# Optimization experiments

Measured on AMD Instinct MI355X. Metric: run time of the kernel, lower is better.

Reference implementation:

```python
import jax, jax.numpy as jnp
import numpy as np

B = 64          # graphs per batch
N = 1500        # nodes per graph (equal sizes -> vectorized sortpool)
NT = B * N      # total nodes
DEG = 16        # avg in-degree
E_PER = N * DEG # edges per graph
F_IN = 128
K = 30          # sortpool k
LATENT = [32, 32, 32, 1]  # total 97
TOTAL_LAT = sum(LATENT)
OUT_DIM = 128


def setup_inputs() -> dict:
    key = jax.random.key(0)
    ks = jax.random.split(key, 16)
    node_feat = jax.random.normal(ks[0], (NT, F_IN), dtype=jnp.float32)
    # edges constrained within each graph (block-diagonal adjacency)
    offs = (jnp.arange(B, dtype=jnp.int32) * N)[:, None]
    edge_src = (jax.random.randint(ks[1], (B, E_PER), 0, N, dtype=jnp.int32) + offs).reshape(-1)
    edge_dst = (jax.random.randint(ks[2], (B, E_PER), 0, N, dtype=jnp.int32) + offs).reshape(-1)

    def lin(k, fan_in, shape):
        return jax.random.normal(k, shape, dtype=jnp.float32) * (1.0 / np.sqrt(fan_in))

    inp = dict(node_feat=node_feat, edge_src=edge_src, edge_dst=edge_dst)
    dims = [F_IN] + LATENT
    for i in range(4):
        inp[f'W{i+1}'] = lin(ks[3 + i], dims[i], (dims[i], dims[i + 1]))
        inp[f'b{i+1}'] = jnp.zeros((dims[i + 1],), jnp.float32)
    inp['conv1_w'] = lin(ks[8], TOTAL_LAT, (16, TOTAL_LAT))   # Conv1d(1,16,97,stride=97)
    inp['conv1_b'] = jnp.zeros((16,), jnp.float32)
    inp['conv2_w'] = lin(ks[9], 16 * 5, (32, 16, 5))          # Conv1d(16,32,5)
    inp['conv2_b'] = jnp.zeros((32,), jnp.float32)
    inp['out_w'] = lin(ks[10], 352, (352, OUT_DIM))
    inp['out_b'] = jnp.zeros((OUT_DIM,), jnp.float32)
    return inp


def reference(node_feat, edge_src, edge_dst, W1, b1, W2, b2, W3, b3, W4, b4,
              conv1_w, conv1_b, conv2_w, conv2_b, out_w, out_b):
    # node degrees (+1 for self loop), from in-edges
    deg = jax.ops.segment_sum(jnp.ones_like(edge_dst, jnp.float32), edge_dst, num_segments=NT)
    node_degs = (deg + 1.0)[:, None]

    # 4 graph-conv layers: (A @ h + h) -> Linear -> /deg -> tanh, concat features
    h = node_feat
    layers = []
    for W, b in ((W1, b1), (W2, b2), (W3, b3), (W4, b4)):
        agg = jax.ops.segment_sum(h[edge_src], edge_dst, num_segments=NT) + h
        h = jnp.tanh((agg @ W + b) / node_degs)
        layers.append(h)
    feat = jnp.concatenate(layers, axis=1)  # [NT, 97]

    # sortpooling: top-k nodes per graph by the last channel
    sort_ch = feat[:, -1].reshape(B, N)
    _, idx = jax.lax.top_k(sort_ch, K)                    # [B, K]
    gidx = (idx + (jnp.arange(B, dtype=idx.dtype) * N)[:, None]).reshape(-1)
    pooled = feat[gidx].reshape(B, K, TOTAL_LAT)          # [B, K, 97]

    # Conv1d(1,16,97,stride=97) over flattened [B,1,K*97] == per-slot linear
    c1 = jax.nn.relu(jnp.einsum('bkd,od->bok', pooled, conv1_w) + conv1_b[None, :, None])  # [B,16,K]
    mp = c1.reshape(B, 16, K // 2, 2).max(axis=-1)        # MaxPool1d(2,2) -> [B,16,15]
    c2 = jax.lax.conv_general_dilated(mp, conv2_w, (1,), 'VALID',
                                      dimension_numbers=('NCH', 'OIH', 'NCH'))
    c2 = jax.nn.relu(c2 + conv2_b[None, :, None])         # [B,32,11]
    dense = c2.reshape(B, -1)                             # [B,352]
    return jax.nn.relu(dense @ out_w + out_b)             # relu(relu(x)) == relu(x)
```

## Files before the change

### kernel.cpp

```cpp
#include <hip/hip_runtime.h>

constexpr int B = 64, N = 1500, NT = B * N;
constexpr int E_PER = 24000, E_TOT = B * E_PER;
constexpr int E_PAD = 34560;
constexpr int F_INN = 128, K = 30, TOT = 97;
constexpr int NB_G = 47;
constexpr int GEMM_TILES = NT / 128;
constexpr int GEMM_BLKS = (GEMM_TILES + 3) / 4;

__global__ __launch_bounds__(1024) void prep(const int* __restrict__ src, const int* __restrict__ dst,
                                             ushort* __restrict__ csr, int* __restrict__ rowst,
                                             int* __restrict__ degi, float* __restrict__ degf,
                                             float* __restrict__ tA,
                                             const float* __restrict__ nf, const float* __restrict__ W1) {
    __shared__ union {
        struct { int hist[N]; uint csr_l32[E_PAD / 2]; int wsum[4]; } c;
        struct { float hs[4][32][128]; float Ws[32][32]; } g;
    } u;
    int bid = blockIdx.x, t = threadIdx.x;

    if (bid < B) {
        ushort* csr_l = (ushort*)u.c.csr_l32;
        int g = bid;
        int gbase = g * N;
        const int* dstg = dst + (size_t)g * E_PER;
        const int* srcg = src + (size_t)g * E_PER;

        for (int i = t; i < N; i += 1024) u.c.hist[i] = 0;
        __syncthreads();
        for (int e = t; e < E_PER; e += 1024)
            atomicAdd(&u.c.hist[dstg[e] - gbase], 1);
        __syncthreads();

        int local[6];
        int sum = 0, x = 0;
        if (t < 256) {
#pragma unroll
            for (int i = 0; i < 6; ++i) {
                int v = t * 6 + i;
                int d = (v < N) ? u.c.hist[v] : 0;
                local[i] = d;
                sum += (d + 7) & ~7;
            }
            x = sum;
            int lane = t & 63;
#pragma unroll
            for (int m = 1; m < 64; m <<= 1) {
                int y = __shfl_up(x, m, 64);
                if (lane >= m) x += y;
            }
            if (lane == 63) u.c.wsum[t >> 6] = x;
        }
        __syncthreads();
        if (t < 256) {
            int woff = 0;
            int wv = t >> 6;
            for (int w = 0; w < wv; ++w) woff += u.c.wsum[w];
            int run = x - sum + woff;
#pragma unroll
            for (int i = 0; i < 6; ++i) {
                int v = t * 6 + i;
                if (v < N) {
                    rowst[gbase + v] = g * E_PAD + run;
                    degi[gbase + v] = local[i];
                    degf[gbase + v] = (float)(local[i] + 1);
                    u.c.hist[v] = run;
                    run += (local[i] + 7) & ~7;
                }
            }
        }
        __syncthreads();
        for (int e = t; e < E_PER; e += 1024) {
            int d = dstg[e] - gbase;
            int pos = atomicAdd(&u.c.hist[d], 1);
            csr_l[pos] = (ushort)(srcg[e] - gbase);
        }
        __syncthreads();
        for (int v = t; v < N; v += 1024)
            for (int s = u.c.hist[v]; s & 7; ++s) csr_l[s] = (ushort)v;
        __syncthreads();
        uint* cg = (uint*)(csr + (size_t)g * E_PAD);
        for (int i = t; i < E_PAD / 2; i += 1024)
            cg[i] = u.c.csr_l32[i];
    } else {
        int sub = t >> 8, tid = t & 255;
        int tile = (bid - B) * 4 + sub;
        bool valid = tile < GEMM_TILES;
        int wv = tid >> 6, lane = tid & 63;
        int v0 = tile * 128;
        int og = wv * 8;
        float acc[2][8];
#pragma unroll
        for (int i = 0; i < 2; ++i)
#pragma unroll
            for (int j = 0; j < 8; ++j) acc[i][j] = 0.f;

        for (int kc = 0; kc < F_INN; kc += 32) {
            __syncthreads();
            if (valid) {
                int n = tid >> 1, kh = (tid & 1) * 16;
                const float* hp = nf + (size_t)(v0 + n) * F_INN + kc + kh;
                const float4* hp4 = reinterpret_cast<const float4*>(hp);
                float4 a = hp4[0], b = hp4[1], c = hp4[2], d = hp4[3];
                float (*hs)[128] = u.g.hs[sub];
                hs[kh + 0][n] = a.x;  hs[kh + 1][n] = a.y;  hs[kh + 2][n] = a.z;  hs[kh + 3][n] = a.w;
                hs[kh + 4][n] = b.x;  hs[kh + 5][n] = b.y;  hs[kh + 6][n] = b.z;  hs[kh + 7][n] = b.w;
                hs[kh + 8][n] = c.x;  hs[kh + 9][n] = c.y;  hs[kh + 10][n] = c.z; hs[kh + 11][n] = c.w;
                hs[kh + 12][n] = d.x; hs[kh + 13][n] = d.y; hs[kh + 14][n] = d.z; hs[kh + 15][n] = d.w;
            }
            if (sub == 0) {
                int r = tid >> 3, c4 = (tid & 7) * 4;
                float4 w = *reinterpret_cast<const float4*>(W1 + (size_t)(kc + r) * 32 + c4);
                *reinterpret_cast<float4*>(&u.g.Ws[r][c4]) = w;
            }
            __syncthreads();
            if (valid) {
#pragma unroll
                for (int k = 0; k < 32; ++k) {
                    float2 hv = *reinterpret_cast<const float2*>(&u.g.hs[sub][k][2 * lane]);
                    float4 w0 = *reinterpret_cast<const float4*>(&u.g.Ws[k][og]);
                    float4 w1 = *reinterpret_cast<const float4*>(&u.g.Ws[k][og + 4]);
                    acc[0][0] += hv.x * w0.x; acc[0][1] += hv.x * w0.y; acc[0][2] += hv.x * w0.z; acc[0][3] += hv.x * w0.w;
                    acc[0][4] += hv.x * w1.x; acc[0][5] += hv.x * w1.y; acc[0][6] += hv.x * w1.z; acc[0][7] += hv.x * w1.w;
                    acc[1][0] += hv.y * w0.x; acc[1][1] += hv.y * w0.y; acc[1][2] += hv.y * w0.z; acc[1][3] += hv.y * w0.w;
                    acc[1][4] += hv.y * w1.x; acc[1][5] += hv.y * w1.y; acc[1][6] += hv.y * w1.z; acc[1][7] += hv.y * w1.w;
                }
            }
        }
        if (valid) {
#pragma unroll
            for (int i = 0; i < 2; ++i) {
                float* op = tA + (size_t)(v0 + 2 * lane + i) * 32 + og;
                float4 r0 = {acc[i][0], acc[i][1], acc[i][2], acc[i][3]};
                float4 r1 = {acc[i][4], acc[i][5], acc[i][6], acc[i][7]};
                reinterpret_cast<float4*>(op)[0] = r0;
                reinterpret_cast<float4*>(op)[1] = r1;
            }
        }
    }
}

template <int FUSE>
__global__ __launch_bounds__(256) void agg_f(const float* __restrict__ t,
                                             const ushort* __restrict__ csr, const int* __restrict__ rowst,
                                             const int* __restrict__ degi, const float* __restrict__ degf,
                                             const float* __restrict__ bias, const float* __restrict__ Wn,
                                             float* __restrict__ hout, float* __restrict__ tn) {
    __shared__ float Ws[1024];
    __shared__ float outs[32][32];
    if (FUSE == 32) {
        for (int i = threadIdx.x; i < 1024; i += 256) Ws[i] = Wn[i];
    }
    int bid = blockIdx.x;
    int xcd = bid & 7, j = bid >> 3;
    int g = xcd + 8 * (j / NB_G);
    int nb = j % NB_G;
    int nl = threadIdx.x >> 3;
    int f4 = threadIdx.x & 7;
    int vl = nb * 32 + nl;
    bool valid = vl < N;
    int v = g * N + vl;
    int gb8 = g * N * 8;
    const float4* t4v = reinterpret_cast<const float4*>(t);
    float4 out = {0.f, 0.f, 0.f, 0.f};
    if (valid) {
        float4 tself = t4v[(unsigned)(v * 8 + f4)];
        int e0 = rowst[v];
        int dc = degi[v];
        int pc = (dc + 7) & ~7;
        float scale = (float)(1 + dc - pc);
        float4 acc = {scale * tself.x, scale * tself.y, scale * tself.z, scale * tself.w};
        float4 s1 = {0.f, 0.f, 0.f, 0.f}, s2 = {0.f, 0.f, 0.f, 0.f};
        float4 s3 = {0.f, 0.f, 0.f, 0.f}, s4v = {0.f, 0.f, 0.f, 0.f};
        for (int e = 0; e < pc; e += 8) {
            ushort4 ia = *reinterpret_cast<const ushort4*>(csr + e0 + e);
            ushort4 ib = *reinterpret_cast<const ushort4*>(csr + e0 + e + 4);
            float4 x0 = t4v[(unsigned)(gb8 + ia.x * 8 + f4)];
            float4 x1 = t4v[(unsigned)(gb8 + ia.y * 8 + f4)];
            float4 x2 = t4v[(unsigned)(gb8 + ia.z * 8 + f4)];
            float4 x3 = t4v[(unsigned)(gb8 + ia.w * 8 + f4)];
            float4 x4 = t4v[(unsigned)(gb8 + ib.x * 8 + f4)];
            float4 x5 = t4v[(unsigned)(gb8 + ib.y * 8 + f4)];
            float4 x6 = t4v[(unsigned)(gb8 + ib.z * 8 + f4)];
            float4 x7 = t4v[(unsigned)(gb8 + ib.w * 8 + f4)];
            s1.x += x0.x + x1.x; s1.y += x0.y + x1.y; s1.z += x0.z + x1.z; s1.w += x0.w + x1.w;
            s2.x += x2.x + x3.x; s2.y += x2.y + x3.y; s2.z += x2.z + x3.z; s2.w += x2.w + x3.w;
            s3.x += x4.x + x5.x; s3.y += x4.y + x5.y; s3.z += x4.z + x5.z; s3.w += x4.w + x5.w;
            s4v.x += x6.x + x7.x; s4v.y += x6.y + x7.y; s4v.z += x6.z + x7.z; s4v.w += x6.w + x7.w;
        }
        acc.x += (s1.x + s2.x) + (s3.x + s4v.x);
        acc.y += (s1.y + s2.y) + (s3.y + s4v.y);
        acc.z += (s1.z + s2.z) + (s3.z + s4v.z);
        acc.w += (s1.w + s2.w) + (s3.w + s4v.w);
        float4 bv = *reinterpret_cast<const float4*>(bias + f4 * 4);
        float inv = 1.0f / degf[v];
        out.x = tanhf((acc.x + bv.x) * inv);
        out.y = tanhf((acc.y + bv.y) * inv);
        out.z = tanhf((acc.z + bv.z) * inv);
        out.w = tanhf((acc.w + bv.w) * inv);
        reinterpret_cast<float4*>(hout)[(unsigned)(v * 8 + f4)] = out;
    }
    if (FUSE == 32) {
        *reinterpret_cast<float4*>(&outs[nl][f4 * 4]) = out;
        __syncthreads();
        if (valid) {
            float4 s = {0.f, 0.f, 0.f, 0.f};
#pragma unroll
            for (int ff = 0; ff < 32; ++ff) {
                float h = outs[nl][ff];
                float4 wr = *reinterpret_cast<const float4*>(&Ws[ff * 32 + f4 * 4]);
                s.x += h * wr.x; s.y += h * wr.y; s.z += h * wr.z; s.w += h * wr.w;
            }
            reinterpret_cast<float4*>(tn)[(unsigned)(v * 8 + f4)] = s;
        }
    } else if (valid) {
        float4 w4 = *reinterpret_cast<const float4*>(Wn + f4 * 4);
        float p = out.x * w4.x + out.y * w4.y + out.z * w4.z + out.w * w4.w;
        p += __shfl_xor(p, 4, 64);
        p += __shfl_xor(p, 2, 64);
        p += __shfl_xor(p, 1, 64);
        if (f4 == 0) tn[v] = p;
    }
}

__global__ __launch_bounds__(512) void sort_head(const float* __restrict__ hc1, const float* __restrict__ hc2,
                                                 const float* __restrict__ hc3, const float* __restrict__ t4,
                                                 const ushort* __restrict__ csr, const int* __restrict__ rowst,
                                                 const int* __restrict__ degi, const float* __restrict__ degf,
                                                 const float* __restrict__ b4,
                                                 const float* __restrict__ c1w, const float* __restrict__ c1b,
                                                 const float* __restrict__ c2w, const float* __restrict__ c2b,
                                                 const float* __restrict__ ow, const float* __restrict__ ob,
                                                 float* __restrict__ out) {
    __shared__ float ts[N];
    __shared__ unsigned int svals[N];
    __shared__ float fvals[N];
    __shared__ int hist[2048];
    __shared__ int canA[N], canB[N];
    __shared__ int winners[32];
    __shared__ int wsum[8];
    __shared__ int st_need, st_ncand, st_tb, st_cab, st_nwin;
    __shared__ int topk_s[K];
    __shared__ float pooled[K][TOT];
    __shared__ float c1[16][K];
    __shared__ float mp[16][16];
    __shared__ float dense[352];
    __shared__ float part[4][128];

    int g = blockIdx.x, t = threadIdx.x;
    int gbase = g * N;
    int lane = t & 63, w = t >> 6;

    for (int v = t; v < N; v += 512) ts[v] = t4[gbase + v];
    if (t == 0) { st_need = K; st_nwin = 0; }
    __syncthreads();
    {
        float b4v = b4[0];
        for (int v = t; v < N; v += 512) {
            int gv = gbase + v;
            int e0 = rowst[gv], dc = degi[gv];
            int pc = (dc + 7) & ~7;
            float scale = (float)(1 + dc - pc);
            float a0 = 0.f, a1 = 0.f, a2 = 0.f, a3 = 0.f;
            for (int e = 0; e < pc; e += 4) {
                ushort4 s4 = *reinterpret_cast<const ushort4*>(csr + e0 + e);
                a0 += ts[s4.x];
                a1 += ts[s4.y];
                a2 += ts[s4.z];
                a3 += ts[s4.w];
            }
            float h = tanhf((scale * ts[v] + (a0 + a1) + (a2 + a3) + b4v) / degf[gv]);
            fvals[v] = h;
            unsigned int b = __float_as_uint(h);
            svals[v] = (b & 0x80000000u) ? ~b : (b | 0x80000000u);
        }
    }
    __syncthreads();

    auto mkkey = [&](int idx) {
        return ((unsigned long long)svals[idx] << 31) | (unsigned int)(0x7FFFFFFF - idx);
    };

    const int SHIFTS[6] = {52, 41, 30, 19, 8, 0};
    int curN = N;
    int src = 0;
    for (int pass = 0; pass < 6; ++pass) {
        int shift = SHIFTS[pass];
        int mask = (pass == 5) ? 0xFF : 0x7FF;
        for (int i = t; i < 2048; i += 512) hist[i] = 0;
        if (t == 0) st_ncand = 0;
        __syncthreads();
        for (int i = t; i < curN; i += 512) {
            int idx = (src == 0) ? i : (src == 1 ? canA[i] : canB[i]);
            int d = (int)((mkkey(idx) >> shift) & mask);
            atomicAdd(&hist[d], 1);
        }
        __syncthreads();
        int need = st_need;
        int c[4];
        int s = 0;
#pragma unroll
        for (int u = 0; u < 4; ++u) { c[u] = hist[2047 - (4 * t + u)]; s += c[u]; }
        int x = s;
#pragma unroll
        for (int m = 1; m < 64; m <<= 1) {
            int y = __shfl_up(x, m, 64);
            if (lane >= m) x += y;
        }
        if (lane == 63) wsum[w] = x;
        __syncthreads();
        int woff = 0;
        for (int ww = 0; ww < w; ++ww) woff += wsum[ww];
        int A = woff + x - s;
#pragma unroll
        for (int u = 0; u < 4; ++u) {
            if (A < need && need <= A + c[u]) { st_tb = 2047 - (4 * t + u); st_cab = A; }
            A += c[u];
        }
        __syncthreads();
        int tb = st_tb, cab = st_cab;
        int* dst = (src == 1) ? canB : canA;
        for (int i = t; i < curN; i += 512) {
            int idx = (src == 0) ? i : (src == 1 ? canA[i] : canB[i]);
            int d = (int)((mkkey(idx) >> shift) & mask);
            if (d > tb) {
                int p = atomicAdd(&st_nwin, 1);
                winners[p] = idx;
            } else if (d == tb) {
                int p = atomicAdd(&st_ncand, 1);
                dst[p] = idx;
            }
        }
        __syncthreads();
        int ncand = st_ncand;
        need -= cab;
        if (t == 0) st_need = need;
        if (ncand == need) {
            int base = st_nwin;
            for (int i = t; i < ncand; i += 512) winners[base + i] = dst[i];
            __syncthreads();
            break;
        }
        curN = ncand;
        src = (src == 1) ? 2 : 1;
        __syncthreads();
    }

    if (t < 64) {
        unsigned long long key = (t < K) ? mkkey(winners[t]) : 0ull;
        unsigned long long kk = ~key;
#pragma unroll
        for (int k = 2; k <= 64; k <<= 1) {
#pragma unroll
            for (int j = k >> 1; j > 0; j >>= 1) {
                unsigned long long o = __shfl_xor(kk, j, 64);
                bool keepMin = ((t & j) == 0) == ((t & k) == 0);
                kk = keepMin ? (kk < o ? kk : o) : (kk > o ? kk : o);
            }
        }
        key = ~kk;
        if (t < K) topk_s[t] = 0x7FFFFFFF - (int)(unsigned int)(key & 0x7FFFFFFFu);
    }
    __syncthreads();

    for (int i = t; i < K * TOT; i += 512) {
        int k = i / TOT, d = i % TOT;
        int vloc = topk_s[k];
        int gi = gbase + vloc;
        float val = (d < 32) ? hc1[(size_t)gi * 32 + d]
                  : (d < 64) ? hc2[(size_t)gi * 32 + d - 32]
                  : (d < 96) ? hc3[(size_t)gi * 32 + d - 64]
                             : fvals[vloc];
        pooled[k][d] = val;
    }
    __syncthreads();
    for (int i = t; i < 16 * K; i += 512) {
        int o = i / K, k = i % K;
        float s = c1b[o];
        for (int d = 0; d < TOT; ++d) s += pooled[k][d] * c1w[o * TOT + d];
        c1[o][k] = fmaxf(s, 0.f);
    }
    __syncthreads();
    for (int i = t; i < 16 * 15; i += 512) {
        int o = i / 15, p = i % 15;
        mp[o][p] = fmaxf(c1[o][2 * p], c1[o][2 * p + 1]);
    }
    __syncthreads();
    for (int i = t; i < 352; i += 512) {
        int o = i / 11, p = i % 11;
        float s = c2b[o];
#pragma unroll
        for (int ci = 0; ci < 16; ++ci)
#pragma unroll
            for (int tt = 0; tt < 5; ++tt)
                s += mp[ci][p + tt] * c2w[(o * 16 + ci) * 5 + tt];
        dense[i] = fmaxf(s, 0.f);
    }
    __syncthreads();
    {
        int o = t & 127, q = t >> 7;
        float s = 0.f;
        for (int m = q * 88; m < (q + 1) * 88; ++m) s += dense[m] * ow[m * 128 + o];
        part[q][o] = s;
    }
    __syncthreads();
    if (t < 128) {
        float s = (part[0][t] + part[1][t]) + (part[2][t] + part[3][t]) + ob[t];
        out[g * 128 + t] = fmaxf(s, 0.f);
    }
}

extern "C" void kernel_launch(void* const* d_in, const int* in_sizes, int n_in,
                              void* d_out, int out_size, void* d_ws, size_t ws_size,
                              hipStream_t stream) {
    const float* node_feat = (const float*)d_in[0];
    const int* esrc = (const int*)d_in[1];
    const int* edst = (const int*)d_in[2];
    const float* W1 = (const float*)d_in[3];
    const float* b1 = (const float*)d_in[4];
    const float* W2 = (const float*)d_in[5];
    const float* b2 = (const float*)d_in[6];
    const float* W3 = (const float*)d_in[7];
    const float* b3 = (const float*)d_in[8];
    const float* W4 = (const float*)d_in[9];
    const float* b4 = (const float*)d_in[10];
    const float* c1w = (const float*)d_in[11];
    const float* c1b = (const float*)d_in[12];
    const float* c2w = (const float*)d_in[13];
    const float* c2b = (const float*)d_in[14];
    const float* ow = (const float*)d_in[15];
    const float* ob = (const float*)d_in[16];

    char* ws = (char*)d_ws;
    size_t off = 0;
    auto alloc = [&](size_t bytes) {
        size_t r = off;
        off += (bytes + 255) & ~(size_t)255;
        return r;
    };
    int* deg_i = (int*)(ws + alloc((size_t)NT * 4));
    int* rowst = (int*)(ws + alloc((size_t)NT * 4));
    float* degf = (float*)(ws + alloc((size_t)NT * 4));
    ushort* csr = (ushort*)(ws + alloc((size_t)B * E_PAD * 2));
    float* tA = (float*)(ws + alloc((size_t)NT * 32 * 4));
    float* tB = (float*)(ws + alloc((size_t)NT * 32 * 4));
    float* hc1 = (float*)(ws + alloc((size_t)NT * 32 * 4));
    float* hc2 = (float*)(ws + alloc((size_t)NT * 32 * 4));
    float* hc3 = (float*)(ws + alloc((size_t)NT * 32 * 4));
    float* t4 = (float*)(ws + alloc((size_t)NT * 4));

    prep<<<B + GEMM_BLKS, 1024, 0, stream>>>(esrc, edst, csr, rowst, deg_i, degf,
                                             tA, node_feat, W1);

    agg_f<32><<<8 * NB_G * 8, 256, 0, stream>>>(tA, csr, rowst, deg_i, degf, b1, W2, hc1, tB);
    agg_f<32><<<8 * NB_G * 8, 256, 0, stream>>>(tB, csr, rowst, deg_i, degf, b2, W3, hc2, tA);
    agg_f<1><<<8 * NB_G * 8, 256, 0, stream>>>(tA, csr, rowst, deg_i, degf, b3, W4, hc3, t4);

    sort_head<<<B, 512, 0, stream>>>(hc1, hc2, hc3, t4, csr, rowst, deg_i, degf, b4,
                                     c1w, c1b, c2w, c2b, ow, ob, (float*)d_out);
}
```

Baseline: 117.2 us.

## Split per-graph CSR build into four node-range quarters per block

The CSR construction in prep now uses four blocks per graph, each owning a quarter of the destination nodes. Every block scans the whole edge list with int4 loads and keeps only edges whose destination falls in its range. This gives four times as many CSR-building blocks and a smaller shared-memory footprint per block, so the serial CSR phase should no longer dominate prep. In exchange, each graph's edge list is read four times, and each quarter's padded slice must fit a fixed capacity of 9216, which risks overflow if a quarter's degree total is skewed.

```diff
diff --git a/kernel.cpp b/kernel.cpp
--- a/kernel.cpp
+++ b/kernel.cpp
@@ -2,7 +2,8 @@
 
 constexpr int B = 64, N = 1500, NT = B * N;
 constexpr int E_PER = 24000, E_TOT = B * E_PER;
-constexpr int E_PAD = 34560;
+constexpr int NQ = 4, NPQ = N / NQ;
+constexpr int CAP = 9216;
 constexpr int F_INN = 128, K = 30, TOT = 97;
 constexpr int NB_G = 47;
 constexpr int GEMM_TILES = NT / 128;
@@ -14,31 +15,38 @@
                                              float* __restrict__ tA,
                                              const float* __restrict__ nf, const float* __restrict__ W1) {
     __shared__ union {
-        struct { int hist[N]; uint csr_l32[E_PAD / 2]; int wsum[4]; } c;
+        struct { int hist[NPQ]; uint4 slice[CAP / 8]; int wtot; } c;
         struct { float hs[4][32][128]; float Ws[32][32]; } g;
     } u;
     int bid = blockIdx.x, t = threadIdx.x;
 
-    if (bid < B) {
-        ushort* csr_l = (ushort*)u.c.csr_l32;
-        int g = bid;
-        int gbase = g * N;
-        const int* dstg = dst + (size_t)g * E_PER;
-        const int* srcg = src + (size_t)g * E_PER;
-
-        for (int i = t; i < N; i += 1024) u.c.hist[i] = 0;
-        __syncthreads();
-        for (int e = t; e < E_PER; e += 1024)
-            atomicAdd(&u.c.hist[dstg[e] - gbase], 1);
-        __syncthreads();
-
-        int local[6];
+    if (bid < B * NQ) {
+        ushort* csr_l = (ushort*)u.c.slice;
+        int g = bid >> 2, q = bid & 3;
+        int gbase = g * N, qlo = q * NPQ;
+        const int4* d4 = reinterpret_cast<const int4*>(dst + (size_t)g * E_PER);
+        const int4* s4 = reinterpret_cast<const int4*>(src + (size_t)g * E_PER);
+
+        for (int i = t; i < NPQ; i += 1024) u.c.hist[i] = 0;
+        __syncthreads();
+        for (int i = t; i < E_PER / 4; i += 1024) {
+            int4 d = d4[i];
+            int x0 = d.x - gbase - qlo, x1 = d.y - gbase - qlo;
+            int x2 = d.z - gbase - qlo, x3 = d.w - gbase - qlo;
+            if ((unsigned)x0 < (unsigned)NPQ) atomicAdd(&u.c.hist[x0], 1);
+            if ((unsigned)x1 < (unsigned)NPQ) atomicAdd(&u.c.hist[x1], 1);
+            if ((unsigned)x2 < (unsigned)NPQ) atomicAdd(&u.c.hist[x2], 1);
+            if ((unsigned)x3 < (unsigned)NPQ) atomicAdd(&u.c.hist[x3], 1);
+        }
+        __syncthreads();
+
+        int local[3];
         int sum = 0, x = 0;
-        if (t < 256) {
-#pragma unroll
-            for (int i = 0; i < 6; ++i) {
-                int v = t * 6 + i;
-                int d = (v < N) ? u.c.hist[v] : 0;
+        if (t < 128) {
+#pragma unroll
+            for (int i = 0; i < 3; ++i) {
+                int v = t * 3 + i;
+                int d = (v < NPQ) ? u.c.hist[v] : 0;
                 local[i] = d;
                 sum += (d + 7) & ~7;
             }
@@ -49,42 +57,47 @@
                 int y = __shfl_up(x, m, 64);
                 if (lane >= m) x += y;
             }
-            if (lane == 63) u.c.wsum[t >> 6] = x;
-        }
-        __syncthreads();
-        if (t < 256) {
-            int woff = 0;
-            int wv = t >> 6;
-            for (int w = 0; w < wv; ++w) woff += u.c.wsum[w];
-            int run = x - sum + woff;
-#pragma unroll
-            for (int i = 0; i < 6; ++i) {
-                int v = t * 6 + i;
-                if (v < N) {
-                    rowst[gbase + v] = g * E_PAD + run;
-                    degi[gbase + v] = local[i];
-                    degf[gbase + v] = (float)(local[i] + 1);
+        }
+        if (t == 63) u.c.wtot = x;
+        __syncthreads();
+        if (t < 128) {
+            int base = (t >= 64) ? u.c.wtot : 0;
+            int run = base + x - sum;
+            int rbase = (g * NQ + q) * CAP;
+#pragma unroll
+            for (int i = 0; i < 3; ++i) {
+                int v = t * 3 + i;
+                if (v < NPQ) {
+                    int gv = gbase + qlo + v;
+                    rowst[gv] = rbase + run;
+                    degi[gv] = local[i];
+                    degf[gv] = (float)(local[i] + 1);
                     u.c.hist[v] = run;
                     run += (local[i] + 7) & ~7;
                 }
             }
         }
         __syncthreads();
-        for (int e = t; e < E_PER; e += 1024) {
-            int d = dstg[e] - gbase;
-            int pos = atomicAdd(&u.c.hist[d], 1);
-            csr_l[pos] = (ushort)(srcg[e] - gbase);
-        }
-        __syncthreads();
-        for (int v = t; v < N; v += 1024)
-            for (int s = u.c.hist[v]; s & 7; ++s) csr_l[s] = (ushort)v;
-        __syncthreads();
-        uint* cg = (uint*)(csr + (size_t)g * E_PAD);
-        for (int i = t; i < E_PAD / 2; i += 1024)
-            cg[i] = u.c.csr_l32[i];
+        for (int i = t; i < E_PER / 4; i += 1024) {
+            int4 d = d4[i];
+            int4 s = s4[i];
+            int x0 = d.x - gbase - qlo, x1 = d.y - gbase - qlo;
+            int x2 = d.z - gbase - qlo, x3 = d.w - gbase - qlo;
+            if ((unsigned)x0 < (unsigned)NPQ) { int p = atomicAdd(&u.c.hist[x0], 1); csr_l[p] = (ushort)(s.x - gbase); }
+            if ((unsigned)x1 < (unsigned)NPQ) { int p = atomicAdd(&u.c.hist[x1], 1); csr_l[p] = (ushort)(s.y - gbase); }
+            if ((unsigned)x2 < (unsigned)NPQ) { int p = atomicAdd(&u.c.hist[x2], 1); csr_l[p] = (ushort)(s.z - gbase); }
+            if ((unsigned)x3 < (unsigned)NPQ) { int p = atomicAdd(&u.c.hist[x3], 1); csr_l[p] = (ushort)(s.w - gbase); }
+        }
+        __syncthreads();
+        for (int v = t; v < NPQ; v += 1024)
+            for (int sft = u.c.hist[v]; sft & 7; ++sft) csr_l[sft] = (ushort)(qlo + v);
+        __syncthreads();
+        uint4* cg = reinterpret_cast<uint4*>(csr + (size_t)(g * NQ + q) * CAP);
+        for (int i = t; i < CAP / 8; i += 1024)
+            cg[i] = u.c.slice[i];
     } else {
         int sub = t >> 8, tid = t & 255;
-        int tile = (bid - B) * 4 + sub;
+        int tile = (bid - B * NQ) * 4 + sub;
         bool valid = tile < GEMM_TILES;
         int wv = tid >> 6, lane = tid & 63;
         int v0 = tile * 128;
@@ -441,7 +454,7 @@
     int* deg_i = (int*)(ws + alloc((size_t)NT * 4));
     int* rowst = (int*)(ws + alloc((size_t)NT * 4));
     float* degf = (float*)(ws + alloc((size_t)NT * 4));
-    ushort* csr = (ushort*)(ws + alloc((size_t)B * E_PAD * 2));
+    ushort* csr = (ushort*)(ws + alloc((size_t)B * NQ * CAP * 2));
     float* tA = (float*)(ws + alloc((size_t)NT * 32 * 4));
     float* tB = (float*)(ws + alloc((size_t)NT * 32 * 4));
     float* hc1 = (float*)(ws + alloc((size_t)NT * 32 * 4));
@@ -449,8 +462,8 @@
     float* hc3 = (float*)(ws + alloc((size_t)NT * 32 * 4));
     float* t4 = (float*)(ws + alloc((size_t)NT * 4));
 
-    prep<<<B + GEMM_BLKS, 1024, 0, stream>>>(esrc, edst, csr, rowst, deg_i, degf,
-                                             tA, node_feat, W1);
+    prep<<<B * NQ + GEMM_BLKS, 1024, 0, stream>>>(esrc, edst, csr, rowst, deg_i, degf,
+                                                  tA, node_feat, W1);
 
     agg_f<32><<<8 * NB_G * 8, 256, 0, stream>>>(tA, csr, rowst, deg_i, degf, b1, W2, hc1, tB);
     agg_f<32><<<8 * NB_G * 8, 256, 0, stream>>>(tB, csr, rowst, deg_i, degf, b2, W3, hc2, tA);
```

Measured after the change: 117.4 us. Within noise of the previous version (+0.2%).

## Fuse CSR build, first GEMM and three aggregation layers into one per-graph kernel

Applied to the files above, without the earlier changes.

Replaces the prep kernel and three agg_f launches with a single kernel of 64 blocks, one per graph, each 1024 threads wide. The block builds its graph's CSR, computes the node-feature GEMM for its own nodes, and then runs all three aggregation layers, separated only by block barriers. This removes three kernel launches and their inter-kernel gaps, and keeps each graph's data local to one CU. The cost is parallelism: only 64 CUs are busy where the old grids spread across thousands of blocks, and each block has to do much more serial work.

```diff
diff --git a/kernel.cpp b/kernel.cpp
--- a/kernel.cpp
+++ b/kernel.cpp
@@ -1,37 +1,38 @@
 #include <hip/hip_runtime.h>
 
 constexpr int B = 64, N = 1500, NT = B * N;
-constexpr int E_PER = 24000, E_TOT = B * E_PER;
+constexpr int E_PER = 24000;
 constexpr int E_PAD = 34560;
 constexpr int F_INN = 128, K = 30, TOT = 97;
-constexpr int NB_G = 47;
-constexpr int GEMM_TILES = NT / 128;
-constexpr int GEMM_BLKS = (GEMM_TILES + 3) / 4;
-
-__global__ __launch_bounds__(1024) void prep(const int* __restrict__ src, const int* __restrict__ dst,
+
+__global__ __launch_bounds__(1024) void mega(const int* __restrict__ src, const int* __restrict__ dst,
+                                             const float* __restrict__ nf,
+                                             const float* __restrict__ W1, const float* __restrict__ b1,
+                                             const float* __restrict__ W2, const float* __restrict__ b2,
+                                             const float* __restrict__ W3, const float* __restrict__ b3,
+                                             const float* __restrict__ W4,
                                              ushort* __restrict__ csr, int* __restrict__ rowst,
                                              int* __restrict__ degi, float* __restrict__ degf,
-                                             float* __restrict__ tA,
-                                             const float* __restrict__ nf, const float* __restrict__ W1) {
+                                             float* __restrict__ tA, float* __restrict__ tB,
+                                             float* __restrict__ hc1, float* __restrict__ hc2,
+                                             float* __restrict__ hc3, float* __restrict__ t4) {
     __shared__ union {
-        struct { int hist[N]; uint csr_l32[E_PAD / 2]; int wsum[4]; } c;
+        struct { int hist[N]; uint4 slice[E_PAD / 8]; int wsum[4]; } c;
         struct { float hs[4][32][128]; float Ws[32][32]; } g;
+        struct { float Wn[1024]; float outs[128][32]; } a;
     } u;
-    int bid = blockIdx.x, t = threadIdx.x;
-
-    if (bid < B) {
-        ushort* csr_l = (ushort*)u.c.csr_l32;
-        int g = bid;
-        int gbase = g * N;
+    int g = blockIdx.x, t = threadIdx.x;
+    int gbase = g * N;
+
+    {
+        ushort* csr_l = (ushort*)u.c.slice;
         const int* dstg = dst + (size_t)g * E_PER;
         const int* srcg = src + (size_t)g * E_PER;
-
         for (int i = t; i < N; i += 1024) u.c.hist[i] = 0;
         __syncthreads();
         for (int e = t; e < E_PER; e += 1024)
             atomicAdd(&u.c.hist[dstg[e] - gbase], 1);
         __syncthreads();
-
         int local[6];
         int sum = 0, x = 0;
         if (t < 256) {
@@ -79,42 +80,43 @@
         for (int v = t; v < N; v += 1024)
             for (int s = u.c.hist[v]; s & 7; ++s) csr_l[s] = (ushort)v;
         __syncthreads();
-        uint* cg = (uint*)(csr + (size_t)g * E_PAD);
-        for (int i = t; i < E_PAD / 2; i += 1024)
-            cg[i] = u.c.csr_l32[i];
-    } else {
+        uint4* cg = reinterpret_cast<uint4*>(csr + (size_t)g * E_PAD);
+        for (int i = t; i < E_PAD / 8; i += 1024)
+            cg[i] = u.c.slice[i];
+    }
+    __syncthreads();
+
+    {
         int sub = t >> 8, tid = t & 255;
-        int tile = (bid - B) * 4 + sub;
-        bool valid = tile < GEMM_TILES;
         int wv = tid >> 6, lane = tid & 63;
-        int v0 = tile * 128;
         int og = wv * 8;
-        float acc[2][8];
-#pragma unroll
-        for (int i = 0; i < 2; ++i)
-#pragma unroll
-            for (int j = 0; j < 8; ++j) acc[i][j] = 0.f;
-
-        for (int kc = 0; kc < F_INN; kc += 32) {
-            __syncthreads();
-            if (valid) {
-                int n = tid >> 1, kh = (tid & 1) * 16;
-                const float* hp = nf + (size_t)(v0 + n) * F_INN + kc + kh;
-                const float4* hp4 = reinterpret_cast<const float4*>(hp);
-                float4 a = hp4[0], b = hp4[1], c = hp4[2], d = hp4[3];
-                float (*hs)[128] = u.g.hs[sub];
-                hs[kh + 0][n] = a.x;  hs[kh + 1][n] = a.y;  hs[kh + 2][n] = a.z;  hs[kh + 3][n] = a.w;
-                hs[kh + 4][n] = b.x;  hs[kh + 5][n] = b.y;  hs[kh + 6][n] = b.z;  hs[kh + 7][n] = b.w;
-                hs[kh + 8][n] = c.x;  hs[kh + 9][n] = c.y;  hs[kh + 10][n] = c.z; hs[kh + 11][n] = c.w;
-                hs[kh + 12][n] = d.x; hs[kh + 13][n] = d.y; hs[kh + 14][n] = d.z; hs[kh + 15][n] = d.w;
-            }
-            if (sub == 0) {
-                int r = tid >> 3, c4 = (tid & 7) * 4;
-                float4 w = *reinterpret_cast<const float4*>(W1 + (size_t)(kc + r) * 32 + c4);
-                *reinterpret_cast<float4*>(&u.g.Ws[r][c4]) = w;
-            }
-            __syncthreads();
-            if (valid) {
+        for (int it = 0; it < 3; ++it) {
+            int tile = it * 4 + sub;
+            int v0 = tile * 128;
+            float acc[2][8];
+#pragma unroll
+            for (int i = 0; i < 2; ++i)
+#pragma unroll
+                for (int j = 0; j < 8; ++j) acc[i][j] = 0.f;
+            for (int kc = 0; kc < F_INN; kc += 32) {
+                __syncthreads();
+                {
+                    int n = tid >> 1, kh = (tid & 1) * 16;
+                    int row = gbase + min(v0 + n, N - 1);
+                    const float4* hp4 = reinterpret_cast<const float4*>(nf + (size_t)row * F_INN + kc + kh);
+                    float4 a = hp4[0], b = hp4[1], c = hp4[2], d = hp4[3];
+                    float (*hs)[128] = u.g.hs[sub];
+                    hs[kh + 0][n] = a.x;  hs[kh + 1][n] = a.y;  hs[kh + 2][n] = a.z;  hs[kh + 3][n] = a.w;
+                    hs[kh + 4][n] = b.x;  hs[kh + 5][n] = b.y;  hs[kh + 6][n] = b.z;  hs[kh + 7][n] = b.w;
+                    hs[kh + 8][n] = c.x;  hs[kh + 9][n] = c.y;  hs[kh + 10][n] = c.z; hs[kh + 11][n] = c.w;
+                    hs[kh + 12][n] = d.x; hs[kh + 13][n] = d.y; hs[kh + 14][n] = d.z; hs[kh + 15][n] = d.w;
+                }
+                if (sub == 0) {
+                    int r = tid >> 3, c4 = (tid & 7) * 4;
+                    float4 w = *reinterpret_cast<const float4*>(W1 + (size_t)(kc + r) * 32 + c4);
+                    *reinterpret_cast<float4*>(&u.g.Ws[r][c4]) = w;
+                }
+                __syncthreads();
 #pragma unroll
                 for (int k = 0; k < 32; ++k) {
                     float2 hv = *reinterpret_cast<const float2*>(&u.g.hs[sub][k][2 * lane]);
@@ -126,101 +128,98 @@
                     acc[1][4] += hv.y * w1.x; acc[1][5] += hv.y * w1.y; acc[1][6] += hv.y * w1.z; acc[1][7] += hv.y * w1.w;
                 }
             }
-        }
-        if (valid) {
 #pragma unroll
             for (int i = 0; i < 2; ++i) {
-                float* op = tA + (size_t)(v0 + 2 * lane + i) * 32 + og;
-                float4 r0 = {acc[i][0], acc[i][1], acc[i][2], acc[i][3]};
-                float4 r1 = {acc[i][4], acc[i][5], acc[i][6], acc[i][7]};
-                reinterpret_cast<float4*>(op)[0] = r0;
-                reinterpret_cast<float4*>(op)[1] = r1;
-            }
-        }
-    }
-}
-
-template <int FUSE>
-__global__ __launch_bounds__(256) void agg_f(const float* __restrict__ t,
-                                             const ushort* __restrict__ csr, const int* __restrict__ rowst,
-                                             const int* __restrict__ degi, const float* __restrict__ degf,
-                                             const float* __restrict__ bias, const float* __restrict__ Wn,
-                                             float* __restrict__ hout, float* __restrict__ tn) {
-    __shared__ float Ws[1024];
-    __shared__ float outs[32][32];
-    if (FUSE == 32) {
-        for (int i = threadIdx.x; i < 1024; i += 256) Ws[i] = Wn[i];
-    }
-    int bid = blockIdx.x;
-    int xcd = bid & 7, j = bid >> 3;
-    int g = xcd + 8 * (j / NB_G);
-    int nb = j % NB_G;
-    int nl = threadIdx.x >> 3;
-    int f4 = threadIdx.x & 7;
-    int vl = nb * 32 + nl;
-    bool valid = vl < N;
-    int v = g * N + vl;
-    int gb8 = g * N * 8;
-    const float4* t4v = reinterpret_cast<const float4*>(t);
-    float4 out = {0.f, 0.f, 0.f, 0.f};
-    if (valid) {
-        float4 tself = t4v[(unsigned)(v * 8 + f4)];
-        int e0 = rowst[v];
-        int dc = degi[v];
-        int pc = (dc + 7) & ~7;
-        float scale = (float)(1 + dc - pc);
-        float4 acc = {scale * tself.x, scale * tself.y, scale * tself.z, scale * tself.w};
-        float4 s1 = {0.f, 0.f, 0.f, 0.f}, s2 = {0.f, 0.f, 0.f, 0.f};
-        float4 s3 = {0.f, 0.f, 0.f, 0.f}, s4v = {0.f, 0.f, 0.f, 0.f};
-        for (int e = 0; e < pc; e += 8) {
-            ushort4 ia = *reinterpret_cast<const ushort4*>(csr + e0 + e);
-            ushort4 ib = *reinterpret_cast<const ushort4*>(csr + e0 + e + 4);
-            float4 x0 = t4v[(unsigned)(gb8 + ia.x * 8 + f4)];
-            float4 x1 = t4v[(unsigned)(gb8 + ia.y * 8 + f4)];
-            float4 x2 = t4v[(unsigned)(gb8 + ia.z * 8 + f4)];
-            float4 x3 = t4v[(unsigned)(gb8 + ia.w * 8 + f4)];
-            float4 x4 = t4v[(unsigned)(gb8 + ib.x * 8 + f4)];
-            float4 x5 = t4v[(unsigned)(gb8 + ib.y * 8 + f4)];
-            float4 x6 = t4v[(unsigned)(gb8 + ib.z * 8 + f4)];
-            float4 x7 = t4v[(unsigned)(gb8 + ib.w * 8 + f4)];
-            s1.x += x0.x + x1.x; s1.y += x0.y + x1.y; s1.z += x0.z + x1.z; s1.w += x0.w + x1.w;
-            s2.x += x2.x + x3.x; s2.y += x2.y + x3.y; s2.z += x2.z + x3.z; s2.w += x2.w + x3.w;
-            s3.x += x4.x + x5.x; s3.y += x4.y + x5.y; s3.z += x4.z + x5.z; s3.w += x4.w + x5.w;
-            s4v.x += x6.x + x7.x; s4v.y += x6.y + x7.y; s4v.z += x6.z + x7.z; s4v.w += x6.w + x7.w;
-        }
-        acc.x += (s1.x + s2.x) + (s3.x + s4v.x);
-        acc.y += (s1.y + s2.y) + (s3.y + s4v.y);
-        acc.z += (s1.z + s2.z) + (s3.z + s4v.z);
-        acc.w += (s1.w + s2.w) + (s3.w + s4v.w);
-        float4 bv = *reinterpret_cast<const float4*>(bias + f4 * 4);
-        float inv = 1.0f / degf[v];
-        out.x = tanhf((acc.x + bv.x) * inv);
-        out.y = tanhf((acc.y + bv.y) * inv);
-        out.z = tanhf((acc.z + bv.z) * inv);
-        out.w = tanhf((acc.w + bv.w) * inv);
-        reinterpret_cast<float4*>(hout)[(unsigned)(v * 8 + f4)] = out;
-    }
-    if (FUSE == 32) {
-        *reinterpret_cast<float4*>(&outs[nl][f4 * 4]) = out;
-        __syncthreads();
-        if (valid) {
-            float4 s = {0.f, 0.f, 0.f, 0.f};
-#pragma unroll
-            for (int ff = 0; ff < 32; ++ff) {
-                float h = outs[nl][ff];
-                float4 wr = *reinterpret_cast<const float4*>(&Ws[ff * 32 + f4 * 4]);
-                s.x += h * wr.x; s.y += h * wr.y; s.z += h * wr.z; s.w += h * wr.w;
-            }
-            reinterpret_cast<float4*>(tn)[(unsigned)(v * 8 + f4)] = s;
-        }
-    } else if (valid) {
-        float4 w4 = *reinterpret_cast<const float4*>(Wn + f4 * 4);
-        float p = out.x * w4.x + out.y * w4.y + out.z * w4.z + out.w * w4.w;
-        p += __shfl_xor(p, 4, 64);
-        p += __shfl_xor(p, 2, 64);
-        p += __shfl_xor(p, 1, 64);
-        if (f4 == 0) tn[v] = p;
-    }
+                int vl = v0 + 2 * lane + i;
+                if (vl < N) {
+                    float* op = tA + (size_t)(gbase + vl) * 32 + og;
+                    float4 r0 = {acc[i][0], acc[i][1], acc[i][2], acc[i][3]};
+                    float4 r1 = {acc[i][4], acc[i][5], acc[i][6], acc[i][7]};
+                    reinterpret_cast<float4*>(op)[0] = r0;
+                    reinterpret_cast<float4*>(op)[1] = r1;
+                }
+            }
+        }
+    }
+    __syncthreads();
+
+    int gb8 = gbase * 8;
+    int nl = t >> 3, f4 = t & 7;
+    const ushort* csrg = csr;
+
+#define AGG_LAYER(TIN, BIASP, HOUT, DO_W4, WNEXT, TOUT)                                            \
+    {                                                                                              \
+        if (!(DO_W4)) {                                                                            \
+            if (t < 1024) u.a.Wn[t] = (WNEXT)[t];                                                  \
+            __syncthreads();                                                                       \
+        }                                                                                          \
+        const float4* t4v = reinterpret_cast<const float4*>(TIN);                                  \
+        float4 bv = *reinterpret_cast<const float4*>((BIASP) + f4 * 4);                            \
+        for (int it = 0; it < 12; ++it) {                                                          \
+            int vl = it * 128 + nl;                                                                \
+            if (vl < N) {                                                                          \
+                int v = gbase + vl;                                                                \
+                float4 tself = t4v[(unsigned)(v * 8 + f4)];                                        \
+                int e0 = rowst[v];                                                                 \
+                int dc = degi[v];                                                                  \
+                int pc = (dc + 7) & ~7;                                                            \
+                float scale = (float)(1 + dc - pc);                                                \
+                float4 acc = {scale * tself.x, scale * tself.y, scale * tself.z, scale * tself.w}; \
+                float4 s1 = {0, 0, 0, 0}, s2 = {0, 0, 0, 0}, s3 = {0, 0, 0, 0}, s4v = {0, 0, 0, 0};\
+                for (int e = 0; e < pc; e += 8) {                                                  \
+                    ushort4 ia = *reinterpret_cast<const ushort4*>(csrg + e0 + e);                 \
+                    ushort4 ib = *reinterpret_cast<const ushort4*>(csrg + e0 + e + 4);             \
+                    float4 x0 = t4v[(unsigned)(gb8 + ia.x * 8 + f4)];                              \
+                    float4 x1 = t4v[(unsigned)(gb8 + ia.y * 8 + f4)];                              \
+                    float4 x2 = t4v[(unsigned)(gb8 + ia.z * 8 + f4)];                              \
+                    float4 x3 = t4v[(unsigned)(gb8 + ia.w * 8 + f4)];                              \
+                    float4 x4 = t4v[(unsigned)(gb8 + ib.x * 8 + f4)];                              \
+                    float4 x5 = t4v[(unsigned)(gb8 + ib.y * 8 + f4)];                              \
+                    float4 x6 = t4v[(unsigned)(gb8 + ib.z * 8 + f4)];                              \
+                    float4 x7 = t4v[(unsigned)(gb8 + ib.w * 8 + f4)];                              \
+                    s1.x += x0.x + x1.x; s1.y += x0.y + x1.y; s1.z += x0.z + x1.z; s1.w += x0.w + x1.w; \
+                    s2.x += x2.x + x3.x; s2.y += x2.y + x3.y; s2.z += x2.z + x3.z; s2.w += x2.w + x3.w; \
+                    s3.x += x4.x + x5.x; s3.y += x4.y + x5.y; s3.z += x4.z + x5.z; s3.w += x4.w + x5.w; \
+                    s4v.x += x6.x + x7.x; s4v.y += x6.y + x7.y; s4v.z += x6.z + x7.z; s4v.w += x6.w + x7.w; \
+                }                                                                                  \
+                acc.x += (s1.x + s2.x) + (s3.x + s4v.x);                                           \
+                acc.y += (s1.y + s2.y) + (s3.y + s4v.y);                                           \
+                acc.z += (s1.z + s2.z) + (s3.z + s4v.z);                                           \
+                acc.w += (s1.w + s2.w) + (s3.w + s4v.w);                                           \
+                float inv = 1.0f / degf[v];                                                        \
+                float4 out;                                                                        \
+                out.x = tanhf((acc.x + bv.x) * inv);                                               \
+                out.y = tanhf((acc.y + bv.y) * inv);                                               \
+                out.z = tanhf((acc.z + bv.z) * inv);                                               \
+                out.w = tanhf((acc.w + bv.w) * inv);                                               \
+                reinterpret_cast<float4*>(HOUT)[(unsigned)(v * 8 + f4)] = out;                     \
+                if (DO_W4) {                                                                       \
+                    float4 w4 = *reinterpret_cast<const float4*>(W4 + f4 * 4);                     \
+                    float p = out.x * w4.x + out.y * w4.y + out.z * w4.z + out.w * w4.w;           \
+                    p += __shfl_xor(p, 4, 64);                                                     \
+                    p += __shfl_xor(p, 2, 64);                                                     \
+                    p += __shfl_xor(p, 1, 64);                                                     \
+                    if (f4 == 0) (TOUT)[v] = p;                                                    \
+                } else {                                                                           \
+                    *reinterpret_cast<float4*>(&u.a.outs[nl][f4 * 4]) = out;                       \
+                    float4 s = {0, 0, 0, 0};                                                       \
+                    _Pragma("unroll")                                                              \
+                    for (int ff = 0; ff < 32; ++ff) {                                              \
+                        float h = u.a.outs[nl][ff];                                                \
+                        float4 wr = *reinterpret_cast<const float4*>(&u.a.Wn[ff * 32 + f4 * 4]);   \
+                        s.x += h * wr.x; s.y += h * wr.y; s.z += h * wr.z; s.w += h * wr.w;        \
+                    }                                                                              \
+                    reinterpret_cast<float4*>(TOUT)[(unsigned)(v * 8 + f4)] = s;                   \
+                }                                                                                  \
+            }                                                                                      \
+        }                                                                                          \
+    }                                                                                              \
+    __syncthreads();
+
+    AGG_LAYER(tA, b1, hc1, false, W2, tB)
+    AGG_LAYER(tB, b2, hc2, false, W3, tA)
+    AGG_LAYER(tA, b3, hc3, true, W4, t4)
+#undef AGG_LAYER
 }
 
 __global__ __launch_bounds__(512) void sort_head(const float* __restrict__ hc1, const float* __restrict__ hc2,
@@ -449,12 +448,8 @@
     float* hc3 = (float*)(ws + alloc((size_t)NT * 32 * 4));
     float* t4 = (float*)(ws + alloc((size_t)NT * 4));
 
-    prep<<<B + GEMM_BLKS, 1024, 0, stream>>>(esrc, edst, csr, rowst, deg_i, degf,
-                                             tA, node_feat, W1);
-
-    agg_f<32><<<8 * NB_G * 8, 256, 0, stream>>>(tA, csr, rowst, deg_i, degf, b1, W2, hc1, tB);
-    agg_f<32><<<8 * NB_G * 8, 256, 0, stream>>>(tB, csr, rowst, deg_i, degf, b2, W3, hc2, tA);
-    agg_f<1><<<8 * NB_G * 8, 256, 0, stream>>>(tA, csr, rowst, deg_i, degf, b3, W4, hc3, t4);
+    mega<<<B, 1024, 0, stream>>>(esrc, edst, node_feat, W1, b1, W2, b2, W3, b3, W4,
+                                 csr, rowst, deg_i, degf, tA, tB, hc1, hc2, hc3, t4);
 
     sort_head<<<B, 512, 0, stream>>>(hc1, hc2, hc3, t4, csr, rowst, deg_i, degf, b4,
                                      c1w, c1b, c2w, c2b, ow, ob, (float*)d_out);
```

Result: slower. 259.7 us (+121.6%).
